# Performance work log

Measured on AMD Instinct MI355X. Metric: run time of the kernel, lower is better.

## Reference

```python
import jax, jax.numpy as jnp
import numpy as np

NUM_EMBEDDINGS = 1024
EMBEDDING_DIM = 256
COMMITMENT_COST = 1.0


def setup_inputs() -> dict:
    key = jax.random.key(0)
    k_in, k_emb = jax.random.split(key)
    inputs = jax.random.normal(k_in, (64, 32, 32, EMBEDDING_DIM), dtype=jnp.float32)
    embeddings = jax.random.normal(k_emb, (NUM_EMBEDDINGS, EMBEDDING_DIM), dtype=jnp.float32)
    return {"inputs": inputs, "embeddings": embeddings}


def reference(inputs, embeddings):
    # Eval-mode forward of VectorQuantizerEMA (EMA buffer update is a no-grad
    # stateful side effect, skipped here; see notes).
    input_shape = inputs.shape
    flat = inputs.reshape(-1, EMBEDDING_DIM)                       # [N, D]
    distances = (
        jnp.sum(flat ** 2, axis=1, keepdims=True)
        + jnp.sum(embeddings ** 2, axis=1)
        - 2.0 * flat @ embeddings.T
    )
    encoding_indices = jnp.argmin(distances, axis=1)               # [N]
    # one-hot @ embeddings == gather (avoid materializing [N, K] one-hot)
    quantized = embeddings[encoding_indices].reshape(input_shape)
    e_latent_loss = jnp.mean((jax.lax.stop_gradient(quantized) - inputs) ** 2)
    loss = COMMITMENT_COST * e_latent_loss
    # straight-through estimator
    quantized_st = inputs + jax.lax.stop_gradient(quantized - inputs)
    return quantized_st, loss, encoding_indices[:, None]
```

## Files before the change

### kernel.cpp

```cpp
#include <hip/hip_runtime.h>
#include <float.h>

#define NROWS 65536
#define DK 256
#define NCODES 1024
#define FLAG_CAP 8192
#define MARGIN1 0.15f
#define D_BIAS 384.0f

#define LOSS_OFF 16777216
#define IDX_OFF  16777217

#define WS_FLAG1   0
#define WS_LOSSP   8
#define WS_ENORMD  520
#define WS_ENORMF  8712
#define WS_FROWS   12808
#define WS_IDX     45576
#define WS_EHI     307728

typedef _Float16 f16x8 __attribute__((ext_vector_type(8)));
typedef float f32x4 __attribute__((ext_vector_type(4)));
typedef unsigned int uint32;

__device__ __forceinline__ uint32 packh2(float a, float b) {
  return (uint32)__builtin_bit_cast(unsigned short, (_Float16)a) |
         ((uint32)__builtin_bit_cast(unsigned short, (_Float16)b) << 16);
}

__global__ __launch_bounds__(256) void init_kernel(
    const float* __restrict__ E, double* __restrict__ enorm_d,
    float* __restrict__ enorm_f, uint4* __restrict__ Ehi,
    int* __restrict__ flag1, double* __restrict__ loss_part) {
  const int t = threadIdx.x;
  const int c = blockIdx.x * 8 + (t >> 5);
  const int g = t & 31;
  if (blockIdx.x == 0) {
    if (t == 0) *flag1 = 0;
    if (t < 64) loss_part[t] = 0.0;
  }
  const float4* er4 = (const float4*)(E + (size_t)c * DK);
  const float4 va = er4[g * 2];
  const float4 vb = er4[g * 2 + 1];
  double s = (double)va.x * va.x + (double)va.y * va.y + (double)va.z * va.z + (double)va.w * va.w
           + (double)vb.x * vb.x + (double)vb.y * vb.y + (double)vb.z * vb.z + (double)vb.w * vb.w;
  uint4 h;
  h.x = packh2(va.x, va.y);
  h.y = packh2(va.z, va.w);
  h.z = packh2(vb.x, vb.y);
  h.w = packh2(vb.z, vb.w);
  const int ctg = c >> 8, cga = (c >> 4) & 15, col = c & 15;
  const int kc = g >> 2, quad = g & 3;
  Ehi[((size_t)((ctg * 8 + kc) * 16 + cga)) * 64 + (size_t)(quad * 16 + col)] = h;
  #pragma unroll
  for (int m = 1; m < 32; m <<= 1) s += __shfl_xor(s, m, 64);
  if (g == 0) {
    enorm_d[c] = s;
    enorm_f[c] = (float)s;
  }
}

__global__ __launch_bounds__(256, 2) void dist_fused(
    const float* __restrict__ X, const uint4* __restrict__ Ehi,
    const float* __restrict__ E, const float* __restrict__ enorm_f,
    int* __restrict__ idx_ws, int* __restrict__ flag1, int* __restrict__ flag_rows,
    float* __restrict__ out, double* __restrict__ loss_part) {
  __shared__ __attribute__((aligned(16))) char lds[32768];
  const int tid = threadIdx.x;
  const int lane = tid & 63;
  const int wid = tid >> 6;
  const int col = lane & 15;
  const int rowBase = blockIdx.x * 64;

  {
    const float4* X4 = (const float4*)X + (size_t)rowBase * 64;
    #pragma unroll
    for (int i = 0; i < 16; ++i) {
      const int f4 = i * 256 + tid;
      const int row = f4 >> 6;
      const int k0 = (f4 & 63) << 2;
      const float4 v = X4[f4];
      uint2 p;
      p.x = packh2(v.x, v.y);
      p.y = packh2(v.z, v.w);
      const int off = (((row >> 4) * 8 + (k0 >> 5)) * 64 + ((k0 >> 3) & 3) * 16 + (row & 15)) * 16
                      + ((k0 >> 2) & 1) * 8;
      *(uint2*)(lds + off) = p;
    }
  }
  __syncthreads();

  float rv1[16], rv2[16];
  #pragma unroll
  for (int i = 0; i < 16; ++i) { rv1[i] = FLT_MAX; rv2[i] = FLT_MAX; }

  for (int ctg = 0; ctg < 4; ++ctg) {
    f32x4 acc[4][4];
    #pragma unroll
    for (int rg = 0; rg < 4; ++rg)
      #pragma unroll
      for (int cg = 0; cg < 4; ++cg) acc[rg][cg] = (f32x4){0.f, 0.f, 0.f, 0.f};

    #pragma unroll 2
    for (int ks = 0; ks < 8; ++ks) {
      const size_t ub = ((size_t)((ctg * 8 + ks) * 16 + wid * 4)) * 64 + (size_t)lane;
      f16x8 a[4], bh[4];
      #pragma unroll
      for (int cg = 0; cg < 4; ++cg) bh[cg] = *(const f16x8*)&Ehi[ub + (size_t)cg * 64];
      #pragma unroll
      for (int rg = 0; rg < 4; ++rg)
        a[rg] = *(const f16x8*)(lds + ((rg * 8 + ks) * 64 + lane) * 16);
      #pragma unroll
      for (int rg = 0; rg < 4; ++rg)
        #pragma unroll
        for (int cg = 0; cg < 4; ++cg)
          acc[rg][cg] = __builtin_amdgcn_mfma_f32_16x16x32_f16(a[rg], bh[cg], acc[rg][cg], 0, 0, 0);
    }
    #pragma unroll
    for (int cg = 0; cg < 4; ++cg) {
      const int code = ctg * 256 + wid * 64 + cg * 16 + col;
      const float en = enorm_f[code] + D_BIAS;
      const uint32 li = (uint32)((ctg << 6) | (cg << 4) | col);
      #pragma unroll
      for (int rg = 0; rg < 4; ++rg)
        #pragma unroll
        for (int reg = 0; reg < 4; ++reg) {
          const int i = rg * 4 + reg;
          const float d = fmaf(-2.0f, acc[rg][cg][reg], en);
          const float p = __builtin_bit_cast(float,
              (__builtin_bit_cast(uint32, d) & 0xFFFFFF00u) | li);
          rv2[i] = fminf(rv2[i], fmaxf(rv1[i], p));
          rv1[i] = fminf(rv1[i], p);
        }
    }
  }

  #pragma unroll
  for (int i = 0; i < 16; ++i) {
    #pragma unroll
    for (int m = 1; m < 16; m <<= 1) {
      const float o1 = __shfl_xor(rv1[i], m, 64);
      const float o2 = __shfl_xor(rv2[i], m, 64);
      rv2[i] = fminf(fminf(rv2[i], o2), fmaxf(rv1[i], o1));
      rv1[i] = fminf(rv1[i], o1);
    }
  }

  __syncthreads();
  float* M = (float*)lds;
  int* idxs = (int*)(lds + 4096);
  if (col == 0) {
    const int quad = lane >> 4;
    #pragma unroll
    for (int i = 0; i < 16; ++i) {
      const int row = (i >> 2) * 16 + quad * 4 + (i & 3);
      M[(row * 4 + wid) * 2 + 0] = rv1[i];
      M[(row * 4 + wid) * 2 + 1] = rv2[i];
    }
  }
  __syncthreads();
  if (tid < 64) {
    const float a1 = M[(tid * 4 + 0) * 2], a2 = M[(tid * 4 + 0) * 2 + 1];
    const float b1 = M[(tid * 4 + 1) * 2], b2 = M[(tid * 4 + 1) * 2 + 1];
    const float c1 = M[(tid * 4 + 2) * 2], c2 = M[(tid * 4 + 2) * 2 + 1];
    const float d1 = M[(tid * 4 + 3) * 2], d2 = M[(tid * 4 + 3) * 2 + 1];
    const float lo1 = fminf(a1, b1), hi1 = fmaxf(a1, b1);
    const float lo2 = fminf(c1, d1), hi2 = fmaxf(c1, d1);
    const float r1 = fminf(lo1, lo2);
    const float s1 = fminf(fmaxf(lo1, lo2), fminf(hi1, hi2));
    const float r2 = fminf(fminf(fminf(a2, b2), fminf(c2, d2)), s1);
    const int w1 = (r1 == a1) ? 0 : (r1 == b1) ? 1 : (r1 == c1) ? 2 : 3;
    const uint32 u1 = __builtin_bit_cast(uint32, r1);
    const int li = (int)(u1 & 255u);
    const int code = ((li >> 6) & 3) * 256 + w1 * 64 + ((li >> 4) & 3) * 16 + (li & 15);
    const int row = rowBase + tid;
    idxs[tid] = code;
    idx_ws[row] = code;
    out[IDX_OFF + row] = (float)code;
    const float q1 = __builtin_bit_cast(float, u1 & 0xFFFFFF00u);
    const float q2 = __builtin_bit_cast(float, __builtin_bit_cast(uint32, r2) & 0xFFFFFF00u);
    if (q2 - q1 < MARGIN1) {
      const int p = atomicAdd(flag1, 1);
      if (p < FLAG_CAP) flag_rows[p] = row;
    }
  }
  __syncthreads();

  const int rsub = tid >> 6, c4 = tid & 63;
  double ls = 0.0;
  #pragma unroll 4
  for (int i = 0; i < 16; ++i) {
    const int rl = i * 4 + rsub;
    const int row = rowBase + rl;
    const int idx = idxs[rl];
    const float4 q = ((const float4*)E)[(size_t)idx * 64 + c4];
    const float4 x = ((const float4*)X)[(size_t)row * 64 + c4];
    ((float4*)out)[(size_t)row * 64 + c4] = q;
    const double d0 = (double)q.x - (double)x.x;
    const double d1 = (double)q.y - (double)x.y;
    const double d2 = (double)q.z - (double)x.z;
    const double d3 = (double)q.w - (double)x.w;
    ls += d0 * d0 + d1 * d1 + d2 * d2 + d3 * d3;
  }
  #pragma unroll
  for (int o = 32; o > 0; o >>= 1) ls += __shfl_down(ls, o, 64);
  __shared__ double wsum[4];
  if ((tid & 63) == 0) wsum[tid >> 6] = ls;
  __syncthreads();
  if (tid == 0)
    atomicAdd(&loss_part[blockIdx.x & 63], wsum[0] + wsum[1] + wsum[2] + wsum[3]);
}

__global__ __launch_bounds__(256) void fixup64(
    const float* __restrict__ X, const float* __restrict__ E,
    const double* __restrict__ enorm_d, const int* __restrict__ flag1,
    const int* __restrict__ flag_rows, const int* __restrict__ idx_ws,
    float* __restrict__ out, double* __restrict__ loss_part) {
  __shared__ float xs[4][256];
  __shared__ double rv[256];
  __shared__ int ri[256];
  __shared__ int rowsh[4], oldsh[4], newsh[4];
  __shared__ double dold_sh[4], dnew_sh[4];
  int cnt = *flag1;
  if (cnt > FLAG_CAP) cnt = FLAG_CAP;
  const int fbase = blockIdx.x * 4;
  if (fbase >= cnt) return;
  const int nr = min(4, cnt - fbase);
  if (threadIdx.x < 4) {
    const int r = threadIdx.x;
    const int row = (r < nr) ? flag_rows[fbase + r] : flag_rows[fbase];
    rowsh[r] = row;
    oldsh[r] = idx_ws[row];
  }
  __syncthreads();
  for (int e = threadIdx.x; e < 4 * 256; e += 256) {
    const int r = e >> 8, k = e & 255;
    xs[r][k] = X[(size_t)rowsh[r] * DK + k];
  }
  __syncthreads();
  double best[4] = {1e300, 1e300, 1e300, 1e300};
  int bi[4] = {0x7fffffff, 0x7fffffff, 0x7fffffff, 0x7fffffff};
  for (int cc = 0; cc < 4; ++cc) {
    const int c = cc * 256 + threadIdx.x;
    const float4* E4 = (const float4*)(E + (size_t)c * DK);
    double s0 = 0.0, s1 = 0.0, s2 = 0.0, s3 = 0.0;
    #pragma unroll 4
    for (int q = 0; q < 64; ++q) {
      const float4 ev = E4[q];
      const float4 x0 = ((const float4*)xs[0])[q];
      const float4 x1 = ((const float4*)xs[1])[q];
      const float4 x2 = ((const float4*)xs[2])[q];
      const float4 x3 = ((const float4*)xs[3])[q];
      s0 += (double)ev.x * x0.x + (double)ev.y * x0.y + (double)ev.z * x0.z + (double)ev.w * x0.w;
      s1 += (double)ev.x * x1.x + (double)ev.y * x1.y + (double)ev.z * x1.z + (double)ev.w * x1.w;
      s2 += (double)ev.x * x2.x + (double)ev.y * x2.y + (double)ev.z * x2.z + (double)ev.w * x2.w;
      s3 += (double)ev.x * x3.x + (double)ev.y * x3.y + (double)ev.z * x3.z + (double)ev.w * x3.w;
    }
    const double en = enorm_d[c];
    const double dd[4] = {en - 2.0 * s0, en - 2.0 * s1, en - 2.0 * s2, en - 2.0 * s3};
    #pragma unroll
    for (int r = 0; r < 4; ++r) {
      if (dd[r] < best[r]) { best[r] = dd[r]; bi[r] = c; }
      if (c == oldsh[r]) dold_sh[r] = dd[r];
    }
  }
  for (int r = 0; r < nr; ++r) {
    rv[threadIdx.x] = best[r];
    ri[threadIdx.x] = bi[r];
    __syncthreads();
    for (int off = 128; off > 0; off >>= 1) {
      if (threadIdx.x < off) {
        const double ov = rv[threadIdx.x + off];
        const int oi = ri[threadIdx.x + off];
        if (ov < rv[threadIdx.x] || (ov == rv[threadIdx.x] && oi < ri[threadIdx.x])) {
          rv[threadIdx.x] = ov;
          ri[threadIdx.x] = oi;
        }
      }
      __syncthreads();
    }
    if (threadIdx.x == 0) { dnew_sh[r] = rv[0]; newsh[r] = ri[0]; }
    __syncthreads();
  }
  for (int r = 0; r < nr; ++r) {
    const int newi = newsh[r];
    if (newi != oldsh[r]) {
      const int row = rowsh[r];
      out[(size_t)row * DK + threadIdx.x] = E[(size_t)newi * DK + threadIdx.x];
      if (threadIdx.x == 0) {
        out[IDX_OFF + row] = (float)newi;
        atomicAdd(&loss_part[row & 63], dnew_sh[r] - dold_sh[r]);
      }
    }
  }
}

__global__ __launch_bounds__(64) void finalize(
    const double* __restrict__ loss_part, float* __restrict__ out) {
  double v = loss_part[threadIdx.x];
  for (int o = 32; o > 0; o >>= 1) v += __shfl_down(v, o, 64);
  if (threadIdx.x == 0) out[LOSS_OFF] = (float)(v / 16777216.0);
}

extern "C" void kernel_launch(void* const* d_in, const int* in_sizes, int n_in,
                              void* d_out, int out_size, void* d_ws, size_t ws_size,
                              hipStream_t stream) {
  const float* X = (const float*)d_in[0];
  const float* E = (const float*)d_in[1];
  float* out = (float*)d_out;
  char* ws = (char*)d_ws;

  int*    flag1     = (int*)(ws + WS_FLAG1);
  double* loss_part = (double*)(ws + WS_LOSSP);
  double* enorm_d   = (double*)(ws + WS_ENORMD);
  float*  enorm_f   = (float*)(ws + WS_ENORMF);
  int*    flag_rows = (int*)(ws + WS_FROWS);
  int*    idx_ws    = (int*)(ws + WS_IDX);
  uint4*  Ehi       = (uint4*)(ws + WS_EHI);

  hipLaunchKernelGGL(init_kernel, dim3(128), dim3(256), 0, stream,
                     E, enorm_d, enorm_f, Ehi, flag1, loss_part);
  hipLaunchKernelGGL(dist_fused, dim3(NROWS / 64), dim3(256), 0, stream,
                     X, Ehi, E, enorm_f, idx_ws, flag1, flag_rows, out, loss_part);
  hipLaunchKernelGGL(fixup64, dim3(FLAG_CAP / 4), dim3(256), 0, stream,
                     X, E, enorm_d, flag1, flag_rows, idx_ws, out, loss_part);
  hipLaunchKernelGGL(finalize, dim3(1), dim3(64), 0, stream, loss_part, out);
}
```

Measured before the change: 236.8 us.

## Add cheap top-2 recheck tier, halve block rows, and prefetch codebook fragments

The distance kernel now handles 32 rows per block with 4-block occupancy and software-prefetches the next codebook MFMA fragment. It tracks the three smallest candidates per row and splits uncertain rows into two tiers. Rows where only the top two are close get a cheap fixup that recomputes those two exact fp64 distances. Rows where the top three are close still get the full 1024-code rescan. Distances are pre-scaled so the margins are tighter, which is meant to cut the expensive fallback work, at the risk of misclassifying near-ties if the fp16 error exceeds the new margins.

```diff
diff --git a/kernel.cpp b/kernel.cpp
--- a/kernel.cpp
+++ b/kernel.cpp
@@ -4,20 +4,25 @@
 #define NROWS 65536
 #define DK 256
 #define NCODES 1024
-#define FLAG_CAP 8192
-#define MARGIN1 0.15f
-#define D_BIAS 384.0f
+#define BLK_ROWS 32
+#define NBLK (NROWS / BLK_ROWS)
+#define FLAG_CAP 16384
+#define FLAG2_CAP 4096
+#define MARGIN_A 0.0025f
+#define MARGIN_B 0.0016f
 
 #define LOSS_OFF 16777216
 #define IDX_OFF  16777217
 
 #define WS_FLAG1   0
+#define WS_FLAG2   4
 #define WS_LOSSP   8
 #define WS_ENORMD  520
 #define WS_ENORMF  8712
 #define WS_FROWS   12808
-#define WS_IDX     45576
-#define WS_EHI     307728
+#define WS_F2ROWS  78344
+#define WS_IDX     94728
+#define WS_EHI     356872
 
 typedef _Float16 f16x8 __attribute__((ext_vector_type(8)));
 typedef float f32x4 __attribute__((ext_vector_type(4)));
@@ -31,12 +36,14 @@
 __global__ __launch_bounds__(256) void init_kernel(
     const float* __restrict__ E, double* __restrict__ enorm_d,
     float* __restrict__ enorm_f, uint4* __restrict__ Ehi,
-    int* __restrict__ flag1, double* __restrict__ loss_part) {
+    int* __restrict__ flag1, int* __restrict__ flag2,
+    double* __restrict__ loss_part) {
   const int t = threadIdx.x;
   const int c = blockIdx.x * 8 + (t >> 5);
   const int g = t & 31;
   if (blockIdx.x == 0) {
     if (t == 0) *flag1 = 0;
+    if (t == 1) *flag2 = 0;
     if (t < 64) loss_part[t] = 0.0;
   }
   const float4* er4 = (const float4*)(E + (size_t)c * DK);
@@ -51,31 +58,34 @@
   h.w = packh2(vb.z, vb.w);
   const int ctg = c >> 8, cga = (c >> 4) & 15, col = c & 15;
   const int kc = g >> 2, quad = g & 3;
-  Ehi[((size_t)((ctg * 8 + kc) * 16 + cga)) * 64 + (size_t)(quad * 16 + col)] = h;
+  Ehi[((size_t)(ctg * 128 + kc * 16 + cga)) * 64 + (size_t)(quad * 16 + col)] = h;
   #pragma unroll
   for (int m = 1; m < 32; m <<= 1) s += __shfl_xor(s, m, 64);
   if (g == 0) {
     enorm_d[c] = s;
-    enorm_f[c] = (float)s;
-  }
-}
-
-__global__ __launch_bounds__(256, 2) void dist_fused(
+    enorm_f[c] = (float)((s + 384.0) * 0.015625);
+  }
+}
+
+__global__ __launch_bounds__(256, 4) void dist_fused(
     const float* __restrict__ X, const uint4* __restrict__ Ehi,
     const float* __restrict__ E, const float* __restrict__ enorm_f,
     int* __restrict__ idx_ws, int* __restrict__ flag1, int* __restrict__ flag_rows,
+    int* __restrict__ flag2, int* __restrict__ flag2_rows,
     float* __restrict__ out, double* __restrict__ loss_part) {
-  __shared__ __attribute__((aligned(16))) char lds[32768];
+  __shared__ __attribute__((aligned(16))) char lds[16384];
+  __shared__ int idxs[BLK_ROWS];
+  __shared__ double wsum[4];
   const int tid = threadIdx.x;
   const int lane = tid & 63;
   const int wid = tid >> 6;
   const int col = lane & 15;
-  const int rowBase = blockIdx.x * 64;
+  const int rowBase = blockIdx.x * BLK_ROWS;
 
   {
     const float4* X4 = (const float4*)X + (size_t)rowBase * 64;
     #pragma unroll
-    for (int i = 0; i < 16; ++i) {
+    for (int i = 0; i < 8; ++i) {
       const int f4 = i * 256 + tid;
       const int row = f4 >> 6;
       const int k0 = (f4 & 63) << 2;
@@ -90,98 +100,133 @@
   }
   __syncthreads();
 
-  float rv1[16], rv2[16];
-  #pragma unroll
-  for (int i = 0; i < 16; ++i) { rv1[i] = FLT_MAX; rv2[i] = FLT_MAX; }
+  float rv1[8], rv2[8], rv3[8];
+  #pragma unroll
+  for (int i = 0; i < 8; ++i) { rv1[i] = FLT_MAX; rv2[i] = FLT_MAX; rv3[i] = FLT_MAX; }
 
   for (int ctg = 0; ctg < 4; ++ctg) {
-    f32x4 acc[4][4];
-    #pragma unroll
-    for (int rg = 0; rg < 4; ++rg)
+    f32x4 acc[2][4];
+    #pragma unroll
+    for (int rg = 0; rg < 2; ++rg)
       #pragma unroll
       for (int cg = 0; cg < 4; ++cg) acc[rg][cg] = (f32x4){0.f, 0.f, 0.f, 0.f};
 
-    #pragma unroll 2
+    const uint4* Bp = Ehi + ((size_t)(ctg * 128 + wid * 4)) * 64 + (size_t)lane;
+    f16x8 bcur[4];
+    #pragma unroll
+    for (int cg = 0; cg < 4; ++cg) bcur[cg] = *(const f16x8*)&Bp[cg * 64];
+    #pragma unroll
     for (int ks = 0; ks < 8; ++ks) {
-      const size_t ub = ((size_t)((ctg * 8 + ks) * 16 + wid * 4)) * 64 + (size_t)lane;
-      f16x8 a[4], bh[4];
+      f16x8 bnxt[4];
+      if (ks < 7) {
+        #pragma unroll
+        for (int cg = 0; cg < 4; ++cg)
+          bnxt[cg] = *(const f16x8*)&Bp[(ks + 1) * 1024 + cg * 64];
+      }
+      f16x8 a[2];
       #pragma unroll
-      for (int cg = 0; cg < 4; ++cg) bh[cg] = *(const f16x8*)&Ehi[ub + (size_t)cg * 64];
-      #pragma unroll
-      for (int rg = 0; rg < 4; ++rg)
+      for (int rg = 0; rg < 2; ++rg)
         a[rg] = *(const f16x8*)(lds + ((rg * 8 + ks) * 64 + lane) * 16);
       #pragma unroll
-      for (int rg = 0; rg < 4; ++rg)
+      for (int rg = 0; rg < 2; ++rg)
         #pragma unroll
         for (int cg = 0; cg < 4; ++cg)
-          acc[rg][cg] = __builtin_amdgcn_mfma_f32_16x16x32_f16(a[rg], bh[cg], acc[rg][cg], 0, 0, 0);
+          acc[rg][cg] = __builtin_amdgcn_mfma_f32_16x16x32_f16(a[rg], bcur[cg], acc[rg][cg], 0, 0, 0);
+      if (ks < 7) {
+        #pragma unroll
+        for (int cg = 0; cg < 4; ++cg) bcur[cg] = bnxt[cg];
+      }
     }
     #pragma unroll
     for (int cg = 0; cg < 4; ++cg) {
       const int code = ctg * 256 + wid * 64 + cg * 16 + col;
-      const float en = enorm_f[code] + D_BIAS;
+      const float en = enorm_f[code];
       const uint32 li = (uint32)((ctg << 6) | (cg << 4) | col);
       #pragma unroll
-      for (int rg = 0; rg < 4; ++rg)
+      for (int rg = 0; rg < 2; ++rg)
         #pragma unroll
         for (int reg = 0; reg < 4; ++reg) {
           const int i = rg * 4 + reg;
-          const float d = fmaf(-2.0f, acc[rg][cg][reg], en);
+          const float d = fmaf(acc[rg][cg][reg], -0.03125f, en);
           const float p = __builtin_bit_cast(float,
               (__builtin_bit_cast(uint32, d) & 0xFFFFFF00u) | li);
-          rv2[i] = fminf(rv2[i], fmaxf(rv1[i], p));
+          const float t1 = fmaxf(rv1[i], p);
           rv1[i] = fminf(rv1[i], p);
+          const float t2 = fmaxf(rv2[i], t1);
+          rv2[i] = fminf(rv2[i], t1);
+          rv3[i] = fminf(rv3[i], t2);
         }
     }
   }
 
   #pragma unroll
-  for (int i = 0; i < 16; ++i) {
+  for (int i = 0; i < 8; ++i) {
     #pragma unroll
     for (int m = 1; m < 16; m <<= 1) {
       const float o1 = __shfl_xor(rv1[i], m, 64);
       const float o2 = __shfl_xor(rv2[i], m, 64);
-      rv2[i] = fminf(fminf(rv2[i], o2), fmaxf(rv1[i], o1));
-      rv1[i] = fminf(rv1[i], o1);
-    }
-  }
-
-  __syncthreads();
-  float* M = (float*)lds;
-  int* idxs = (int*)(lds + 4096);
+      const float o3 = __shfl_xor(rv3[i], m, 64);
+      const float hi = fmaxf(rv1[i], o1);
+      const float n1 = fminf(rv1[i], o1);
+      const float c = fminf(rv2[i], o2);
+      const float d = fmaxf(rv2[i], o2);
+      rv1[i] = n1;
+      rv2[i] = fminf(hi, c);
+      rv3[i] = fminf(fminf(fmaxf(hi, c), d), fminf(rv3[i], o3));
+    }
+  }
+
+  __syncthreads();
+  uint32* M = (uint32*)lds;
   if (col == 0) {
     const int quad = lane >> 4;
     #pragma unroll
-    for (int i = 0; i < 16; ++i) {
+    for (int i = 0; i < 8; ++i) {
       const int row = (i >> 2) * 16 + quad * 4 + (i & 3);
-      M[(row * 4 + wid) * 2 + 0] = rv1[i];
-      M[(row * 4 + wid) * 2 + 1] = rv2[i];
-    }
-  }
-  __syncthreads();
-  if (tid < 64) {
-    const float a1 = M[(tid * 4 + 0) * 2], a2 = M[(tid * 4 + 0) * 2 + 1];
-    const float b1 = M[(tid * 4 + 1) * 2], b2 = M[(tid * 4 + 1) * 2 + 1];
-    const float c1 = M[(tid * 4 + 2) * 2], c2 = M[(tid * 4 + 2) * 2 + 1];
-    const float d1 = M[(tid * 4 + 3) * 2], d2 = M[(tid * 4 + 3) * 2 + 1];
-    const float lo1 = fminf(a1, b1), hi1 = fmaxf(a1, b1);
-    const float lo2 = fminf(c1, d1), hi2 = fmaxf(c1, d1);
-    const float r1 = fminf(lo1, lo2);
-    const float s1 = fminf(fmaxf(lo1, lo2), fminf(hi1, hi2));
-    const float r2 = fminf(fminf(fminf(a2, b2), fminf(c2, d2)), s1);
-    const int w1 = (r1 == a1) ? 0 : (r1 == b1) ? 1 : (r1 == c1) ? 2 : 3;
-    const uint32 u1 = __builtin_bit_cast(uint32, r1);
-    const int li = (int)(u1 & 255u);
-    const int code = ((li >> 6) & 3) * 256 + w1 * 64 + ((li >> 4) & 3) * 16 + (li & 15);
+      const uint32 u1 = __builtin_bit_cast(uint32, rv1[i]);
+      const uint32 u2 = __builtin_bit_cast(uint32, rv2[i]);
+      const uint32 li1 = u1 & 255u, li2 = u2 & 255u;
+      uint32* Mr = &M[(row * 4 + wid) * 5];
+      Mr[0] = u1;
+      Mr[1] = (uint32)(((li1 >> 6) & 3) * 256 + wid * 64 + ((li1 >> 4) & 3) * 16 + (li1 & 15));
+      Mr[2] = u2;
+      Mr[3] = (uint32)(((li2 >> 6) & 3) * 256 + wid * 64 + ((li2 >> 4) & 3) * 16 + (li2 & 15));
+      Mr[4] = __builtin_bit_cast(uint32, rv3[i]);
+    }
+  }
+  __syncthreads();
+  if (tid < BLK_ROWS) {
+    float b1 = FLT_MAX, b2 = FLT_MAX, b3 = FLT_MAX;
+    int bi1 = 0, bi2 = 0;
+    #pragma unroll
+    for (int w = 0; w < 4; ++w) {
+      const uint32* Mr = &M[(tid * 4 + w) * 5];
+      const float v1 = __builtin_bit_cast(float, Mr[0]);
+      const float v2 = __builtin_bit_cast(float, Mr[2]);
+      const float v3 = __builtin_bit_cast(float, Mr[4]);
+      const int g1 = (int)Mr[1], g2 = (int)Mr[3];
+      if (v1 < b1) { b3 = b2; b2 = b1; bi2 = bi1; b1 = v1; bi1 = g1; }
+      else if (v1 < b2) { b3 = b2; b2 = v1; bi2 = g1; }
+      else b3 = fminf(b3, v1);
+      if (v2 < b1) { b3 = b2; b2 = b1; bi2 = bi1; b1 = v2; bi1 = g2; }
+      else if (v2 < b2) { b3 = b2; b2 = v2; bi2 = g2; }
+      else b3 = fminf(b3, v2);
+      b3 = fminf(b3, v3);
+    }
     const int row = rowBase + tid;
-    idxs[tid] = code;
-    idx_ws[row] = code;
-    out[IDX_OFF + row] = (float)code;
-    const float q1 = __builtin_bit_cast(float, u1 & 0xFFFFFF00u);
-    const float q2 = __builtin_bit_cast(float, __builtin_bit_cast(uint32, r2) & 0xFFFFFF00u);
-    if (q2 - q1 < MARGIN1) {
+    idxs[tid] = bi1;
+    idx_ws[row] = bi1;
+    out[IDX_OFF + row] = (float)bi1;
+    const float q1 = __builtin_bit_cast(float, __builtin_bit_cast(uint32, b1) & 0xFFFFFF00u);
+    const float q2 = __builtin_bit_cast(float, __builtin_bit_cast(uint32, b2) & 0xFFFFFF00u);
+    const float q3 = __builtin_bit_cast(float, __builtin_bit_cast(uint32, b3) & 0xFFFFFF00u);
+    if (q2 - q1 < MARGIN_A) {
       const int p = atomicAdd(flag1, 1);
-      if (p < FLAG_CAP) flag_rows[p] = row;
+      if (p < FLAG_CAP) flag_rows[p] = row | (bi2 << 16);
+    }
+    if (q3 - q1 < MARGIN_B) {
+      const int p = atomicAdd(flag2, 1);
+      if (p < FLAG2_CAP) flag2_rows[p] = row;
     }
   }
   __syncthreads();
@@ -189,7 +234,7 @@
   const int rsub = tid >> 6, c4 = tid & 63;
   double ls = 0.0;
   #pragma unroll 4
-  for (int i = 0; i < 16; ++i) {
+  for (int i = 0; i < 8; ++i) {
     const int rl = i * 4 + rsub;
     const int row = rowBase + rl;
     const int idx = idxs[rl];
@@ -204,93 +249,106 @@
   }
   #pragma unroll
   for (int o = 32; o > 0; o >>= 1) ls += __shfl_down(ls, o, 64);
-  __shared__ double wsum[4];
   if ((tid & 63) == 0) wsum[tid >> 6] = ls;
   __syncthreads();
   if (tid == 0)
     atomicAdd(&loss_part[blockIdx.x & 63], wsum[0] + wsum[1] + wsum[2] + wsum[3]);
 }
 
+__global__ __launch_bounds__(256) void fixupA(
+    const float* __restrict__ X, const float* __restrict__ E,
+    const double* __restrict__ enorm_d, const int* __restrict__ flag1,
+    const int* __restrict__ flag_rows, int* __restrict__ idx_ws,
+    float* __restrict__ out, double* __restrict__ loss_part) {
+  int cnt = *flag1;
+  if (cnt > FLAG_CAP) cnt = FLAG_CAP;
+  const int r = blockIdx.x * 4 + (threadIdx.x >> 6);
+  if (r >= cnt) return;
+  const int lane = threadIdx.x & 63;
+  const uint32 rec = (uint32)flag_rows[r];
+  const int row = (int)(rec & 0xFFFFu);
+  const int c2 = (int)(rec >> 16);
+  const int c1 = idx_ws[row];
+  const float4 xv = ((const float4*)X)[(size_t)row * 64 + lane];
+  const float4 e1 = ((const float4*)E)[(size_t)c1 * 64 + lane];
+  const float4 e2 = ((const float4*)E)[(size_t)c2 * 64 + lane];
+  double s1 = (double)xv.x * e1.x + (double)xv.y * e1.y + (double)xv.z * e1.z + (double)xv.w * e1.w;
+  double s2 = (double)xv.x * e2.x + (double)xv.y * e2.y + (double)xv.z * e2.z + (double)xv.w * e2.w;
+  #pragma unroll
+  for (int o = 32; o > 0; o >>= 1) {
+    s1 += __shfl_down(s1, o, 64);
+    s2 += __shfl_down(s2, o, 64);
+  }
+  s1 = __shfl(s1, 0, 64);
+  s2 = __shfl(s2, 0, 64);
+  const double d1 = enorm_d[c1] - 2.0 * s1;
+  const double d2 = enorm_d[c2] - 2.0 * s2;
+  if (d2 < d1 || (d2 == d1 && c2 < c1)) {
+    ((float4*)out)[(size_t)row * 64 + lane] = e2;
+    if (lane == 0) {
+      idx_ws[row] = c2;
+      out[IDX_OFF + row] = (float)c2;
+      atomicAdd(&loss_part[row & 63], d2 - d1);
+    }
+  }
+}
+
 __global__ __launch_bounds__(256) void fixup64(
     const float* __restrict__ X, const float* __restrict__ E,
-    const double* __restrict__ enorm_d, const int* __restrict__ flag1,
-    const int* __restrict__ flag_rows, const int* __restrict__ idx_ws,
+    const double* __restrict__ enorm_d, const int* __restrict__ flag2,
+    const int* __restrict__ flag2_rows, int* __restrict__ idx_ws,
     float* __restrict__ out, double* __restrict__ loss_part) {
-  __shared__ float xs[4][256];
+  __shared__ float xs[256];
   __shared__ double rv[256];
   __shared__ int ri[256];
-  __shared__ int rowsh[4], oldsh[4], newsh[4];
-  __shared__ double dold_sh[4], dnew_sh[4];
-  int cnt = *flag1;
-  if (cnt > FLAG_CAP) cnt = FLAG_CAP;
-  const int fbase = blockIdx.x * 4;
-  if (fbase >= cnt) return;
-  const int nr = min(4, cnt - fbase);
-  if (threadIdx.x < 4) {
-    const int r = threadIdx.x;
-    const int row = (r < nr) ? flag_rows[fbase + r] : flag_rows[fbase];
-    rowsh[r] = row;
-    oldsh[r] = idx_ws[row];
-  }
-  __syncthreads();
-  for (int e = threadIdx.x; e < 4 * 256; e += 256) {
-    const int r = e >> 8, k = e & 255;
-    xs[r][k] = X[(size_t)rowsh[r] * DK + k];
-  }
-  __syncthreads();
-  double best[4] = {1e300, 1e300, 1e300, 1e300};
-  int bi[4] = {0x7fffffff, 0x7fffffff, 0x7fffffff, 0x7fffffff};
+  __shared__ double dold_s;
+  __shared__ int old_s;
+  int cnt = *flag2;
+  if (cnt > FLAG2_CAP) cnt = FLAG2_CAP;
+  if ((int)blockIdx.x >= cnt) return;
+  const int row = flag2_rows[blockIdx.x];
+  const int t = threadIdx.x;
+  if (t == 0) old_s = idx_ws[row];
+  xs[t] = X[(size_t)row * DK + t];
+  __syncthreads();
+  const int old = old_s;
+  double best = 1e300;
+  int bi = 0x7fffffff;
+  double dold = 0.0;
+  #pragma unroll
   for (int cc = 0; cc < 4; ++cc) {
-    const int c = cc * 256 + threadIdx.x;
+    const int c = cc * 256 + t;
     const float4* E4 = (const float4*)(E + (size_t)c * DK);
-    double s0 = 0.0, s1 = 0.0, s2 = 0.0, s3 = 0.0;
+    double s = 0.0;
     #pragma unroll 4
     for (int q = 0; q < 64; ++q) {
       const float4 ev = E4[q];
-      const float4 x0 = ((const float4*)xs[0])[q];
-      const float4 x1 = ((const float4*)xs[1])[q];
-      const float4 x2 = ((const float4*)xs[2])[q];
-      const float4 x3 = ((const float4*)xs[3])[q];
-      s0 += (double)ev.x * x0.x + (double)ev.y * x0.y + (double)ev.z * x0.z + (double)ev.w * x0.w;
-      s1 += (double)ev.x * x1.x + (double)ev.y * x1.y + (double)ev.z * x1.z + (double)ev.w * x1.w;
-      s2 += (double)ev.x * x2.x + (double)ev.y * x2.y + (double)ev.z * x2.z + (double)ev.w * x2.w;
-      s3 += (double)ev.x * x3.x + (double)ev.y * x3.y + (double)ev.z * x3.z + (double)ev.w * x3.w;
-    }
-    const double en = enorm_d[c];
-    const double dd[4] = {en - 2.0 * s0, en - 2.0 * s1, en - 2.0 * s2, en - 2.0 * s3};
-    #pragma unroll
-    for (int r = 0; r < 4; ++r) {
-      if (dd[r] < best[r]) { best[r] = dd[r]; bi[r] = c; }
-      if (c == oldsh[r]) dold_sh[r] = dd[r];
-    }
-  }
-  for (int r = 0; r < nr; ++r) {
-    rv[threadIdx.x] = best[r];
-    ri[threadIdx.x] = bi[r];
+      const float4 xq = ((const float4*)xs)[q];
+      s += (double)ev.x * xq.x + (double)ev.y * xq.y + (double)ev.z * xq.z + (double)ev.w * xq.w;
+    }
+    const double d = enorm_d[c] - 2.0 * s;
+    if (d < best) { best = d; bi = c; }
+    if (c == old) dold = d;
+  }
+  rv[t] = best;
+  ri[t] = bi;
+  if (t == (old & 255)) dold_s = dold;
+  __syncthreads();
+  for (int off = 128; off > 0; off >>= 1) {
+    if (t < off) {
+      const double ov = rv[t + off];
+      const int oi = ri[t + off];
+      if (ov < rv[t] || (ov == rv[t] && oi < ri[t])) { rv[t] = ov; ri[t] = oi; }
+    }
     __syncthreads();
-    for (int off = 128; off > 0; off >>= 1) {
-      if (threadIdx.x < off) {
-        const double ov = rv[threadIdx.x + off];
-        const int oi = ri[threadIdx.x + off];
-        if (ov < rv[threadIdx.x] || (ov == rv[threadIdx.x] && oi < ri[threadIdx.x])) {
-          rv[threadIdx.x] = ov;
-          ri[threadIdx.x] = oi;
-        }
-      }
-      __syncthreads();
-    }
-    if (threadIdx.x == 0) { dnew_sh[r] = rv[0]; newsh[r] = ri[0]; }
-    __syncthreads();
-  }
-  for (int r = 0; r < nr; ++r) {
-    const int newi = newsh[r];
-    if (newi != oldsh[r]) {
-      const int row = rowsh[r];
-      out[(size_t)row * DK + threadIdx.x] = E[(size_t)newi * DK + threadIdx.x];
-      if (threadIdx.x == 0) {
-        out[IDX_OFF + row] = (float)newi;
-        atomicAdd(&loss_part[row & 63], dnew_sh[r] - dold_sh[r]);
-      }
+  }
+  const int newi = ri[0];
+  if (newi != old) {
+    out[(size_t)row * DK + t] = E[(size_t)newi * DK + t];
+    if (t == 0) {
+      idx_ws[row] = newi;
+      out[IDX_OFF + row] = (float)newi;
+      atomicAdd(&loss_part[row & 63], rv[0] - dold_s);
     }
   }
 }
@@ -310,19 +368,24 @@
   float* out = (float*)d_out;
   char* ws = (char*)d_ws;
 
-  int*    flag1     = (int*)(ws + WS_FLAG1);
-  double* loss_part = (double*)(ws + WS_LOSSP);
-  double* enorm_d   = (double*)(ws + WS_ENORMD);
-  float*  enorm_f   = (float*)(ws + WS_ENORMF);
-  int*    flag_rows = (int*)(ws + WS_FROWS);
-  int*    idx_ws    = (int*)(ws + WS_IDX);
-  uint4*  Ehi       = (uint4*)(ws + WS_EHI);
+  int*    flag1      = (int*)(ws + WS_FLAG1);
+  int*    flag2      = (int*)(ws + WS_FLAG2);
+  double* loss_part  = (double*)(ws + WS_LOSSP);
+  double* enorm_d    = (double*)(ws + WS_ENORMD);
+  float*  enorm_f    = (float*)(ws + WS_ENORMF);
+  int*    flag_rows  = (int*)(ws + WS_FROWS);
+  int*    flag2_rows = (int*)(ws + WS_F2ROWS);
+  int*    idx_ws     = (int*)(ws + WS_IDX);
+  uint4*  Ehi        = (uint4*)(ws + WS_EHI);
 
   hipLaunchKernelGGL(init_kernel, dim3(128), dim3(256), 0, stream,
-                     E, enorm_d, enorm_f, Ehi, flag1, loss_part);
-  hipLaunchKernelGGL(dist_fused, dim3(NROWS / 64), dim3(256), 0, stream,
-                     X, Ehi, E, enorm_f, idx_ws, flag1, flag_rows, out, loss_part);
-  hipLaunchKernelGGL(fixup64, dim3(FLAG_CAP / 4), dim3(256), 0, stream,
+                     E, enorm_d, enorm_f, Ehi, flag1, flag2, loss_part);
+  hipLaunchKernelGGL(dist_fused, dim3(NBLK), dim3(256), 0, stream,
+                     X, Ehi, E, enorm_f, idx_ws, flag1, flag_rows,
+                     flag2, flag2_rows, out, loss_part);
+  hipLaunchKernelGGL(fixupA, dim3(FLAG_CAP / 4), dim3(256), 0, stream,
                      X, E, enorm_d, flag1, flag_rows, idx_ws, out, loss_part);
+  hipLaunchKernelGGL(fixup64, dim3(FLAG2_CAP), dim3(256), 0, stream,
+                     X, E, enorm_d, flag2, flag2_rows, idx_ws, out, loss_part);
   hipLaunchKernelGGL(finalize, dim3(1), dim3(64), 0, stream, loss_part, out);
 }
```

After: 257.5 us. 1.09x slower.
